# Performance work log

Measured on AMD Instinct MI355X. Metric: run time of the kernel, lower is better.

## Reference

```python
import jax, jax.numpy as jnp
import numpy as np

B, N, S = 8, 512, 96
SD = TD = H = 256
NH, HD = 8, 32  # num_heads, head_dim
OUT = 4


def setup_inputs() -> dict:
    key = jax.random.key(0)
    ks = jax.random.split(key, 20)
    g = lambda k, shape: (jax.random.normal(k, shape, dtype=jnp.float32) * 0.02)
    return {
        "spatial_features": jax.random.normal(ks[0], (B, N, SD), dtype=jnp.float32),
        "temporal_features": jax.random.normal(ks[1], (B, S, TD), dtype=jnp.float32),
        "Ws": g(ks[2], (H, SD)),   "bs": g(ks[3], (H,)),
        "Wt": g(ks[4], (H, TD)),   "bt": g(ks[5], (H,)),
        "Win": g(ks[6], (3 * H, H)), "bin": g(ks[7], (3 * H,)),
        "Wao": g(ks[8], (H, H)),   "bao": g(ks[9], (H,)),
        "W1": g(ks[10], (H, H)),   "b1": g(ks[11], (H,)),
        "Wo1": g(ks[12], (H // 2, H)), "bo1": g(ks[13], (H // 2,)),
        "Wo2": g(ks[14], (OUT, H // 2)), "bo2": g(ks[15], (OUT,)),
    }


def reference(spatial_features, temporal_features, Ws, bs, Wt, bt, Win, bin, Wao, bao,
              W1, b1, Wo1, bo1, Wo2, bo2):
    # Projections
    sp = spatial_features @ Ws.T + bs          # [B, N, H]
    tp = temporal_features @ Wt.T + bt         # [B, S, H]
    # MultiheadAttention in_proj (batched over all N node-queries at once;
    # mathematically identical to the original per-node loop)
    Wq, Wk, Wv = Win[:H], Win[H:2 * H], Win[2 * H:]
    bq, bk, bv = bin[:H], bin[H:2 * H], bin[2 * H:]
    q = (sp @ Wq.T + bq).reshape(B, N, NH, HD)   # [B, N, h, d]
    k = (tp @ Wk.T + bk).reshape(B, S, NH, HD)   # [B, S, h, d]
    v = (tp @ Wv.T + bv).reshape(B, S, NH, HD)
    scale = 1.0 / np.sqrt(HD).astype(np.float32)
    logits = jnp.einsum('bnhd,bshd->bhns', q * scale, k)   # [B, h, N, S]
    attn = jax.nn.softmax(logits, axis=-1)
    ctx = jnp.einsum('bhns,bshd->bnhd', attn, v).reshape(B, N, H)
    attended = ctx @ Wao.T + bao               # [B, N, H] (out_proj)
    # fusion_layer: Linear + ReLU (dropout=identity in eval)
    fused = jax.nn.relu(attended @ W1.T + b1)  # [B, N, H]
    # output_layer: Linear -> ReLU -> Linear
    h2 = jax.nn.relu(fused @ Wo1.T + bo1)      # [B, N, H/2]
    y = h2 @ Wo2.T + bo2                       # [B, N, OUT]
    # original expands over seq_len BEFORE fusion_layer; since all layers are
    # pointwise over the (S, N) grid, compute once per node and broadcast.
    return jnp.broadcast_to(y[:, None, :, :], (B, S, N, OUT))
```

## Files before the change

kernel.cpp:

```cpp
#include <hip/hip_runtime.h>

#define BB 8
#define NN 512
#define SS 96
#define HH 256
#define NHD 8
#define HDD 32
#define OUTD 4

#define WSB_OFF  0
#define WQB_OFF  65536
#define WAOB_OFF 131072
#define W1B_OFF  196608
#define WO1B_OFF 262144
#define CAST_TOTAL 294912
#define KB_OFF   294912
#define VTB_OFF  491520

typedef __attribute__((ext_vector_type(8))) short bf16x8;
typedef __attribute__((ext_vector_type(4))) float f32x4;

__device__ __forceinline__ unsigned short f2bf(float f) {
    unsigned int u = __float_as_uint(f);
    u = (u + 0x7FFFu + ((u >> 16) & 1u)) >> 16;
    return (unsigned short)u;
}

__device__ __forceinline__ bf16x8 ldw8(const float* __restrict__ p) {
    float4 a = *(const float4*)p, b = *(const float4*)(p + 4);
    bf16x8 r;
    r[0] = (short)f2bf(a.x); r[1] = (short)f2bf(a.y);
    r[2] = (short)f2bf(a.z); r[3] = (short)f2bf(a.w);
    r[4] = (short)f2bf(b.x); r[5] = (short)f2bf(b.y);
    r[6] = (short)f2bf(b.z); r[7] = (short)f2bf(b.w);
    return r;
}

template<int NCT>
__device__ __forceinline__ void mfma_stage(
    const unsigned short* __restrict__ Asw,
    const unsigned short* __restrict__ Wb,
    int lane, int wave, f32x4 acc[NCT])
{
    const int row = lane & 15, kq = lane >> 4;
    #pragma unroll
    for (int ct = 0; ct < NCT; ++ct) acc[ct] = (f32x4){0.f, 0.f, 0.f, 0.f};
    #pragma unroll 2
    for (int kt = 0; kt < 8; ++kt) {
        const int slot = kt * 4 + kq;
        bf16x8 a = *(const bf16x8*)(Asw + row * 256 + ((slot ^ (row & 7)) << 3));
        #pragma unroll
        for (int ct = 0; ct < NCT; ++ct) {
            const unsigned short* wp =
                Wb + (size_t)((wave * NCT + ct) * 16 + row) * 256 + kt * 32 + kq * 8;
            bf16x8 b = *(const bf16x8*)wp;
            acc[ct] = __builtin_amdgcn_mfma_f32_16x16x32_bf16(a, b, acc[ct], 0, 0, 0);
        }
    }
}

template<int NCT>
__device__ __forceinline__ void mfma_stage_f32w(
    const unsigned short* __restrict__ Asw,
    const float* __restrict__ Wf,
    int lane, int wave, f32x4 acc[NCT])
{
    const int row = lane & 15, kq = lane >> 4;
    #pragma unroll
    for (int ct = 0; ct < NCT; ++ct) acc[ct] = (f32x4){0.f, 0.f, 0.f, 0.f};
    #pragma unroll 2
    for (int kt = 0; kt < 8; ++kt) {
        const int slot = kt * 4 + kq;
        bf16x8 a = *(const bf16x8*)(Asw + row * 256 + ((slot ^ (row & 7)) << 3));
        #pragma unroll
        for (int ct = 0; ct < NCT; ++ct) {
            const float* wp =
                Wf + (size_t)((wave * NCT + ct) * 16 + row) * 256 + kt * 32 + kq * 8;
            bf16x8 b = ldw8(wp);
            acc[ct] = __builtin_amdgcn_mfma_f32_16x16x32_bf16(a, b, acc[ct], 0, 0, 0);
        }
    }
}

template<int NCT, bool RELU>
__device__ __forceinline__ void epi_lds(
    unsigned short* __restrict__ OutSw, const float* __restrict__ bias,
    int lane, int wave, const f32x4 acc[NCT])
{
    const int col0 = lane & 15, rq = lane >> 4;
    #pragma unroll
    for (int ct = 0; ct < NCT; ++ct) {
        const int C = wave * NCT * 16 + ct * 16 + col0;
        const float bb = bias[C];
        const int slot = C >> 3, within = C & 7;
        #pragma unroll
        for (int r = 0; r < 4; ++r) {
            const int R = rq * 4 + r;
            float v = acc[ct][r] + bb;
            if (RELU) v = fmaxf(v, 0.f);
            OutSw[R * 256 + ((slot ^ (R & 7)) << 3) + within] = f2bf(v);
        }
    }
}

template<int NCT>
__device__ __forceinline__ void epi_gbf16(
    unsigned short* __restrict__ Og, const float* __restrict__ bias,
    int lane, int wave, const f32x4 acc[NCT])
{
    const int col0 = lane & 15, rq = lane >> 4;
    #pragma unroll
    for (int ct = 0; ct < NCT; ++ct) {
        const int C = wave * NCT * 16 + ct * 16 + col0;
        const float bb = bias[C];
        #pragma unroll
        for (int r = 0; r < 4; ++r) {
            const int R = rq * 4 + r;
            Og[(size_t)R * 256 + C] = f2bf(acc[ct][r] + bb);
        }
    }
}

__device__ __forceinline__ void stage_A(
    const float* __restrict__ Ag, unsigned short* __restrict__ Asw, int tid)
{
    #pragma unroll
    for (int ii = 0; ii < 4; ++ii) {
        int i = tid + ii * 256;
        int row = i >> 6, c4 = i & 63;
        float4 v = ((const float4*)(Ag + (size_t)row * 256))[c4];
        int col = c4 * 4;
        int slot = col >> 3, half = (col >> 2) & 1;
        ushort4 o;
        o.x = f2bf(v.x); o.y = f2bf(v.y); o.z = f2bf(v.z); o.w = f2bf(v.w);
        *(ushort4*)(Asw + row * 256 + ((slot ^ (row & 7)) << 3) + half * 4) = o;
    }
}

__global__ __launch_bounds__(256) void k_prep(
    const float* __restrict__ temporal,
    const float* __restrict__ bt, const float* __restrict__ bin,
    const float* __restrict__ Wt, const float* __restrict__ Win,
    const float* __restrict__ Ws, const float* __restrict__ Wao,
    const float* __restrict__ W1, const float* __restrict__ Wo1,
    unsigned short* __restrict__ kb, unsigned short* __restrict__ vtb,
    unsigned short* __restrict__ bfw)
{
    const int tid = threadIdx.x;
    if (blockIdx.x < 192) {
        __shared__ __align__(16) unsigned short A0[16 * 256];
        __shared__ __align__(16) unsigned short MID[16 * 256];
        const int lane = tid & 63, wave = tid >> 6;
        const int m = blockIdx.x >> 2;
        const int c = blockIdx.x & 3;
        const int r0 = m * 16;
        f32x4 acc[4];
        stage_A(temporal + (size_t)r0 * 256, A0, tid);
        __syncthreads();
        mfma_stage_f32w<4>(A0, Wt, lane, wave, acc);
        epi_lds<4, false>(MID, bt, lane, wave, acc);
        __syncthreads();
        f32x4 a2[2];
        if (c < 2) {
            mfma_stage_f32w<2>(MID, Win + (size_t)(256 + c * 128) * 256, lane, wave, a2);
            epi_gbf16<2>(kb + (size_t)r0 * 256 + c * 128, bin + 256 + c * 128,
                         lane, wave, a2);
        } else {
            mfma_stage_f32w<2>(MID, Win + (size_t)(512 + (c - 2) * 128) * 256, lane, wave, a2);
            const int bb_ = r0 / 96, s0 = r0 % 96;
            const int col0 = lane & 15, rq = lane >> 4;
            #pragma unroll
            for (int ct = 0; ct < 2; ++ct) {
                const int Cl = (c - 2) * 128 + wave * 32 + ct * 16 + col0;
                const float bv = bin[512 + Cl];
                #pragma unroll
                for (int r = 0; r < 4; ++r) {
                    const int R = rq * 4 + r;
                    vtb[((size_t)(bb_ * 256 + Cl)) * 96 + s0 + R] = f2bf(a2[ct][r] + bv);
                }
            }
        }
    } else {
        int idx = (blockIdx.x - 192) * 256 + tid;
        for (int j4 = idx; j4 < CAST_TOTAL / 4; j4 += 48 * 256) {
            int e = j4 * 4;
            const float* src; int off;
            if (e < 65536)       { src = Ws;  off = e; }
            else if (e < 131072) { src = Win; off = e - 65536; }
            else if (e < 196608) { src = Wao; off = e - 131072; }
            else if (e < 262144) { src = W1;  off = e - 196608; }
            else                 { src = Wo1; off = e - 262144; }
            float4 v = *(const float4*)(src + off);
            ushort4 o;
            o.x = f2bf(v.x); o.y = f2bf(v.y); o.z = f2bf(v.z); o.w = f2bf(v.w);
            *(ushort4*)(bfw + e) = o;
        }
    }
}

__global__ __launch_bounds__(256) void k_main(
    const float* __restrict__ spatial,
    const float* __restrict__ bs, const float* __restrict__ bin,
    const unsigned short* __restrict__ bfw,
    const unsigned short* __restrict__ kb, const unsigned short* __restrict__ vtb,
    const float* __restrict__ bao, const float* __restrict__ b1,
    const float* __restrict__ bo1,
    const float* __restrict__ Wo2, const float* __restrict__ bo2,
    float* __restrict__ out)
{
    __shared__ __align__(16) unsigned short A0[16 * 256];
    __shared__ __align__(16) unsigned short MID[16 * 256];
    __shared__ __align__(16) unsigned short Q[16 * 256];
    __shared__ __align__(16) unsigned short P[4][16 * 104];
    __shared__ __align__(16) float H2[16 * 128];
    __shared__ __align__(16) float y[16][OUTD];
    const int tid = threadIdx.x, lane = tid & 63, wave = tid >> 6;
    const int b = blockIdx.x >> 5;
    const int n0 = (blockIdx.x & 31) * 16;
    const int cl = lane & 15, kq = lane >> 4;
    const float scale = 0.17677669529663687f;
    f32x4 acc[4];

    stage_A(spatial + (size_t)(b * NN + n0) * 256, A0, tid);
    __syncthreads();
    mfma_stage<4>(A0, bfw + WSB_OFF, lane, wave, acc);
    epi_lds<4, false>(MID, bs, lane, wave, acc);
    __syncthreads();
    mfma_stage<4>(MID, bfw + WQB_OFF, lane, wave, acc);
    epi_lds<4, false>(Q, bin, lane, wave, acc);

    unsigned short* Pw = &P[wave][0];
    #pragma unroll
    for (int hh = 0; hh < 2; ++hh) {
        const int h = wave * 2 + hh;
        const int slotq = h * 4 + kq;
        bf16x8 aq = *(const bf16x8*)(Q + cl * 256 + ((slotq ^ (cl & 7)) << 3));
        f32x4 l[6];
        #pragma unroll
        for (int t = 0; t < 6; ++t) {
            bf16x8 bk = *(const bf16x8*)(kb + (size_t)(b * SS + t * 16 + cl) * 256 + h * 32 + kq * 8);
            l[t] = __builtin_amdgcn_mfma_f32_16x16x32_bf16(aq, bk, (f32x4){0.f,0.f,0.f,0.f}, 0, 0, 0);
        }
        float pr[6][4];
        float sum[4] = {0.f, 0.f, 0.f, 0.f};
        #pragma unroll
        for (int t = 0; t < 6; ++t)
            #pragma unroll
            for (int r = 0; r < 4; ++r) {
                float p = __expf(l[t][r] * scale);
                pr[t][r] = p; sum[r] += p;
            }
        #pragma unroll
        for (int r = 0; r < 4; ++r) {
            float s = sum[r];
            s += __shfl_xor(s, 1); s += __shfl_xor(s, 2);
            s += __shfl_xor(s, 4); s += __shfl_xor(s, 8);
            sum[r] = 1.0f / s;
        }
        #pragma unroll
        for (int t = 0; t < 6; ++t)
            #pragma unroll
            for (int r = 0; r < 4; ++r)
                Pw[(kq * 4 + r) * 104 + t * 16 + cl] = f2bf(pr[t][r] * sum[r]);
        f32x4 c0 = (f32x4){0.f,0.f,0.f,0.f}, c1 = (f32x4){0.f,0.f,0.f,0.f};
        #pragma unroll
        for (int ks = 0; ks < 3; ++ks) {
            bf16x8 pa = *(const bf16x8*)(Pw + cl * 104 + ks * 32 + kq * 8);
            bf16x8 v0 = *(const bf16x8*)(vtb + (size_t)(b * 256 + h * 32 + cl) * 96 + ks * 32 + kq * 8);
            bf16x8 v1 = *(const bf16x8*)(vtb + (size_t)(b * 256 + h * 32 + 16 + cl) * 96 + ks * 32 + kq * 8);
            c0 = __builtin_amdgcn_mfma_f32_16x16x32_bf16(pa, v0, c0, 0, 0, 0);
            c1 = __builtin_amdgcn_mfma_f32_16x16x32_bf16(pa, v1, c1, 0, 0, 0);
        }
        #pragma unroll
        for (int dt = 0; dt < 2; ++dt) {
            const f32x4 cc = dt ? c1 : c0;
            const int C = h * 32 + dt * 16 + cl;
            const int slot = C >> 3, within = C & 7;
            #pragma unroll
            for (int r = 0; r < 4; ++r) {
                const int R = kq * 4 + r;
                A0[R * 256 + ((slot ^ (R & 7)) << 3) + within] = f2bf(cc[r]);
            }
        }
    }
    __syncthreads();

    mfma_stage<4>(A0, bfw + WAOB_OFF, lane, wave, acc);
    epi_lds<4, false>(MID, bao, lane, wave, acc);
    __syncthreads();
    mfma_stage<4>(MID, bfw + W1B_OFF, lane, wave, acc);
    epi_lds<4, true>(A0, b1, lane, wave, acc);
    __syncthreads();
    {
        f32x4 a2[2];
        mfma_stage<2>(A0, bfw + WO1B_OFF, lane, wave, a2);
        const int rq = lane >> 4;
        #pragma unroll
        for (int ct = 0; ct < 2; ++ct) {
            const int C = wave * 32 + ct * 16 + cl;
            const float bb = bo1[C];
            #pragma unroll
            for (int r = 0; r < 4; ++r) {
                const int R = rq * 4 + r;
                H2[R * 128 + C] = fmaxf(a2[ct][r] + bb, 0.f);
            }
        }
    }
    __syncthreads();
    if (tid < 64) {
        int r = tid >> 2, o = tid & 3;
        float a = 0.f;
        const float4* w4 = (const float4*)(Wo2 + (size_t)o * 128);
        const float4* h4 = (const float4*)(H2 + r * 128);
        for (int kk = 0; kk < 32; ++kk) {
            float4 w = w4[kk], hv = h4[kk];
            a += hv.x * w.x + hv.y * w.y + hv.z * w.z + hv.w * w.w;
        }
        y[r][o] = a + bo2[o];
    }
    __syncthreads();
    for (int i = tid; i < 16 * SS; i += 256) {
        int s = i >> 4;
        int r = i & 15;
        *(float4*)(out + ((size_t)(b * SS + s) * NN + (n0 + r)) * OUTD) = *(const float4*)y[r];
    }
}

extern "C" void kernel_launch(void* const* d_in, const int* in_sizes, int n_in,
                              void* d_out, int out_size, void* d_ws, size_t ws_size,
                              hipStream_t stream) {
    const float* spatial  = (const float*)d_in[0];
    const float* temporal = (const float*)d_in[1];
    const float* Ws  = (const float*)d_in[2];
    const float* bs  = (const float*)d_in[3];
    const float* Wt  = (const float*)d_in[4];
    const float* bt  = (const float*)d_in[5];
    const float* Win = (const float*)d_in[6];
    const float* bin = (const float*)d_in[7];
    const float* Wao = (const float*)d_in[8];
    const float* bao = (const float*)d_in[9];
    const float* W1  = (const float*)d_in[10];
    const float* b1  = (const float*)d_in[11];
    const float* Wo1 = (const float*)d_in[12];
    const float* bo1 = (const float*)d_in[13];
    const float* Wo2 = (const float*)d_in[14];
    const float* bo2 = (const float*)d_in[15];
    float* out = (float*)d_out;
    unsigned short* wsu = (unsigned short*)d_ws;

    unsigned short* bfw = wsu;
    unsigned short* kb  = wsu + KB_OFF;
    unsigned short* vtb = wsu + VTB_OFF;

    hipLaunchKernelGGL(k_prep, dim3(240), dim3(256), 0, stream,
                       temporal, bt, bin, Wt, Win, Ws, Wao, W1, Wo1,
                       kb, vtb, bfw);
    hipLaunchKernelGGL(k_main, dim3(256), dim3(256), 0, stream,
                       spatial, bs, bin, bfw, kb, vtb,
                       bao, b1, bo1, Wo2, bo2, out);
}
```

Measured before the change: 126.1 us.

## Double threads per block to eight waves, splitting column tiles and heads per wave

Both kernels now run 512-thread blocks (8 waves), with each wave computing half as many 16-column MFMA tiles and one attention head instead of two. The goal is more latency hiding and more MFMA parallelism per CU, since the grid (256 blocks) barely fills the device. The cast section of k_prep is resized to 24 blocks of 512 threads. In exchange it doubles the per-block P buffer in LDS and adds more waves contending at each barrier, and the fixed-work tails (the Wo2 dot and output broadcast) stay as they were.

```diff
diff --git a/kernel.cpp b/kernel.cpp
--- a/kernel.cpp
+++ b/kernel.cpp
@@ -121,12 +121,13 @@
     }
 }
 
+template<int NT>
 __device__ __forceinline__ void stage_A(
     const float* __restrict__ Ag, unsigned short* __restrict__ Asw, int tid)
 {
     #pragma unroll
-    for (int ii = 0; ii < 4; ++ii) {
-        int i = tid + ii * 256;
+    for (int ii = 0; ii < 1024 / NT; ++ii) {
+        int i = tid + ii * NT;
         int row = i >> 6, c4 = i & 63;
         float4 v = ((const float4*)(Ag + (size_t)row * 256))[c4];
         int col = c4 * 4;
@@ -137,7 +138,7 @@
     }
 }
 
-__global__ __launch_bounds__(256) void k_prep(
+__global__ __launch_bounds__(512) void k_prep(
     const float* __restrict__ temporal,
     const float* __restrict__ bt, const float* __restrict__ bin,
     const float* __restrict__ Wt, const float* __restrict__ Win,
@@ -154,35 +155,32 @@
         const int m = blockIdx.x >> 2;
         const int c = blockIdx.x & 3;
         const int r0 = m * 16;
-        f32x4 acc[4];
-        stage_A(temporal + (size_t)r0 * 256, A0, tid);
+        f32x4 acc[2];
+        stage_A<512>(temporal + (size_t)r0 * 256, A0, tid);
         __syncthreads();
-        mfma_stage_f32w<4>(A0, Wt, lane, wave, acc);
-        epi_lds<4, false>(MID, bt, lane, wave, acc);
+        mfma_stage_f32w<2>(A0, Wt, lane, wave, acc);
+        epi_lds<2, false>(MID, bt, lane, wave, acc);
         __syncthreads();
-        f32x4 a2[2];
+        f32x4 a1[1];
         if (c < 2) {
-            mfma_stage_f32w<2>(MID, Win + (size_t)(256 + c * 128) * 256, lane, wave, a2);
-            epi_gbf16<2>(kb + (size_t)r0 * 256 + c * 128, bin + 256 + c * 128,
-                         lane, wave, a2);
+            mfma_stage_f32w<1>(MID, Win + (size_t)(256 + c * 128) * 256, lane, wave, a1);
+            epi_gbf16<1>(kb + (size_t)r0 * 256 + c * 128, bin + 256 + c * 128,
+                         lane, wave, a1);
         } else {
-            mfma_stage_f32w<2>(MID, Win + (size_t)(512 + (c - 2) * 128) * 256, lane, wave, a2);
+            mfma_stage_f32w<1>(MID, Win + (size_t)(512 + (c - 2) * 128) * 256, lane, wave, a1);
             const int bb_ = r0 / 96, s0 = r0 % 96;
             const int col0 = lane & 15, rq = lane >> 4;
+            const int Cl = (c - 2) * 128 + wave * 16 + col0;
+            const float bv = bin[512 + Cl];
             #pragma unroll
-            for (int ct = 0; ct < 2; ++ct) {
-                const int Cl = (c - 2) * 128 + wave * 32 + ct * 16 + col0;
-                const float bv = bin[512 + Cl];
-                #pragma unroll
-                for (int r = 0; r < 4; ++r) {
-                    const int R = rq * 4 + r;
-                    vtb[((size_t)(bb_ * 256 + Cl)) * 96 + s0 + R] = f2bf(a2[ct][r] + bv);
-                }
+            for (int r = 0; r < 4; ++r) {
+                const int R = rq * 4 + r;
+                vtb[((size_t)(bb_ * 256 + Cl)) * 96 + s0 + R] = f2bf(a1[0][r] + bv);
             }
         }
     } else {
-        int idx = (blockIdx.x - 192) * 256 + tid;
-        for (int j4 = idx; j4 < CAST_TOTAL / 4; j4 += 48 * 256) {
+        int idx = (blockIdx.x - 192) * 512 + tid;
+        for (int j4 = idx; j4 < CAST_TOTAL / 4; j4 += 24 * 512) {
             int e = j4 * 4;
             const float* src; int off;
             if (e < 65536)       { src = Ws;  off = e; }
@@ -198,7 +196,7 @@
     }
 }
 
-__global__ __launch_bounds__(256) void k_main(
+__global__ __launch_bounds__(512) void k_main(
     const float* __restrict__ spatial,
     const float* __restrict__ bs, const float* __restrict__ bin,
     const unsigned short* __restrict__ bfw,
@@ -211,7 +209,7 @@
     __shared__ __align__(16) unsigned short A0[16 * 256];
     __shared__ __align__(16) unsigned short MID[16 * 256];
     __shared__ __align__(16) unsigned short Q[16 * 256];
-    __shared__ __align__(16) unsigned short P[4][16 * 104];
+    __shared__ __align__(16) unsigned short P[8][16 * 104];
     __shared__ __align__(16) float H2[16 * 128];
     __shared__ __align__(16) float y[16][OUTD];
     const int tid = threadIdx.x, lane = tid & 63, wave = tid >> 6;
@@ -219,20 +217,19 @@
     const int n0 = (blockIdx.x & 31) * 16;
     const int cl = lane & 15, kq = lane >> 4;
     const float scale = 0.17677669529663687f;
-    f32x4 acc[4];
-
-    stage_A(spatial + (size_t)(b * NN + n0) * 256, A0, tid);
-    __syncthreads();
-    mfma_stage<4>(A0, bfw + WSB_OFF, lane, wave, acc);
-    epi_lds<4, false>(MID, bs, lane, wave, acc);
-    __syncthreads();
-    mfma_stage<4>(MID, bfw + WQB_OFF, lane, wave, acc);
-    epi_lds<4, false>(Q, bin, lane, wave, acc);
+    f32x4 acc[2];
+
+    stage_A<512>(spatial + (size_t)(b * NN + n0) * 256, A0, tid);
+    __syncthreads();
+    mfma_stage<2>(A0, bfw + WSB_OFF, lane, wave, acc);
+    epi_lds<2, false>(MID, bs, lane, wave, acc);
+    __syncthreads();
+    mfma_stage<2>(MID, bfw + WQB_OFF, lane, wave, acc);
+    epi_lds<2, false>(Q, bin, lane, wave, acc);
 
     unsigned short* Pw = &P[wave][0];
-    #pragma unroll
-    for (int hh = 0; hh < 2; ++hh) {
-        const int h = wave * 2 + hh;
+    {
+        const int h = wave;
         const int slotq = h * 4 + kq;
         bf16x8 aq = *(const bf16x8*)(Q + cl * 256 + ((slotq ^ (cl & 7)) << 3));
         f32x4 l[6];
@@ -285,25 +282,22 @@
     }
     __syncthreads();
 
-    mfma_stage<4>(A0, bfw + WAOB_OFF, lane, wave, acc);
-    epi_lds<4, false>(MID, bao, lane, wave, acc);
-    __syncthreads();
-    mfma_stage<4>(MID, bfw + W1B_OFF, lane, wave, acc);
-    epi_lds<4, true>(A0, b1, lane, wave, acc);
+    mfma_stage<2>(A0, bfw + WAOB_OFF, lane, wave, acc);
+    epi_lds<2, false>(MID, bao, lane, wave, acc);
+    __syncthreads();
+    mfma_stage<2>(MID, bfw + W1B_OFF, lane, wave, acc);
+    epi_lds<2, true>(A0, b1, lane, wave, acc);
     __syncthreads();
     {
-        f32x4 a2[2];
-        mfma_stage<2>(A0, bfw + WO1B_OFF, lane, wave, a2);
+        f32x4 a1[1];
+        mfma_stage<1>(A0, bfw + WO1B_OFF, lane, wave, a1);
         const int rq = lane >> 4;
-        #pragma unroll
-        for (int ct = 0; ct < 2; ++ct) {
-            const int C = wave * 32 + ct * 16 + cl;
-            const float bb = bo1[C];
-            #pragma unroll
-            for (int r = 0; r < 4; ++r) {
-                const int R = rq * 4 + r;
-                H2[R * 128 + C] = fmaxf(a2[ct][r] + bb, 0.f);
-            }
+        const int C = wave * 16 + cl;
+        const float bb = bo1[C];
+        #pragma unroll
+        for (int r = 0; r < 4; ++r) {
+            const int R = rq * 4 + r;
+            H2[R * 128 + C] = fmaxf(a1[0][r] + bb, 0.f);
         }
     }
     __syncthreads();
@@ -319,7 +313,7 @@
         y[r][o] = a + bo2[o];
     }
     __syncthreads();
-    for (int i = tid; i < 16 * SS; i += 256) {
+    for (int i = tid; i < 16 * SS; i += 512) {
         int s = i >> 4;
         int r = i & 15;
         *(float4*)(out + ((size_t)(b * SS + s) * NN + (n0 + r)) * OUTD) = *(const float4*)y[r];
@@ -352,10 +346,10 @@
     unsigned short* kb  = wsu + KB_OFF;
     unsigned short* vtb = wsu + VTB_OFF;
 
-    hipLaunchKernelGGL(k_prep, dim3(240), dim3(256), 0, stream,
+    hipLaunchKernelGGL(k_prep, dim3(216), dim3(512), 0, stream,
                        temporal, bt, bin, Wt, Win, Ws, Wao, W1, Wo1,
                        kb, vtb, bfw);
-    hipLaunchKernelGGL(k_main, dim3(256), dim3(256), 0, stream,
+    hipLaunchKernelGGL(k_main, dim3(256), dim3(512), 0, stream,
                        spatial, bs, bin, bfw, kb, vtb,
                        bao, b1, bo1, Wo2, bo2, out);
 }
```

After: 123.3 us. -2.2%, faster.
